# Performance work log

Hardware: AMD Instinct MI355X
Metric: run time of the kernel (lower is better)

## Reference

```python
import jax, jax.numpy as jnp
import numpy as np

N_NODES = 100000
N_EDGES = 1600000
N_GRAPHS = 256
F_IN = 38
HID = 64


def graph_conv(x, edge_index, w_rel, b_rel, w_root):
    # PyG GraphConv (aggr='add'): out = lin_rel(sum_{j in N(i)} x_j) + lin_root(x_i)
    src, dst = edge_index[0], edge_index[1]
    agg = jax.ops.segment_sum(x[src], dst, num_segments=N_NODES)  # [N, F]
    return agg @ w_rel + b_rel + x @ w_root


def setup_inputs() -> dict:
    key = jax.random.key(0)
    ks = jax.random.split(key, 10)
    x = jax.random.normal(ks[0], (N_NODES, F_IN), dtype=jnp.float32)
    edge_index = jax.random.randint(ks[1], (2, N_EDGES), 0, N_NODES, dtype=jnp.int64)
    batch = jnp.sort(jax.random.randint(ks[2], (N_NODES,), 0, N_GRAPHS, dtype=jnp.int64))
    s1 = 1.0 / np.sqrt(F_IN)
    s2 = 1.0 / np.sqrt(HID)
    w1_rel = jax.random.uniform(ks[3], (F_IN, HID), jnp.float32, -s1, s1)
    b1_rel = jax.random.uniform(ks[4], (HID,), jnp.float32, -s1, s1)
    w1_root = jax.random.uniform(ks[5], (F_IN, HID), jnp.float32, -s1, s1)
    w2_rel = jax.random.uniform(ks[6], (HID, HID), jnp.float32, -s2, s2)
    b2_rel = jax.random.uniform(ks[7], (HID,), jnp.float32, -s2, s2)
    w2_root = jax.random.uniform(ks[8], (HID, HID), jnp.float32, -s2, s2)
    return {"x": x, "edge_index": edge_index, "batch": batch,
            "w1_rel": w1_rel, "b1_rel": b1_rel, "w1_root": w1_root,
            "w2_rel": w2_rel, "b2_rel": b2_rel, "w2_root": w2_root}


def reference(x, edge_index, batch, w1_rel, b1_rel, w1_root, w2_rel, b2_rel, w2_root):
    h = graph_conv(x, edge_index, w1_rel, b1_rel, w1_root)
    h = jax.nn.relu(h)
    h = graph_conv(h, edge_index, w2_rel, b2_rel, w2_root)
    # global_mean_pool: segment mean over batch ids
    sums = jax.ops.segment_sum(h, batch, num_segments=N_GRAPHS)  # [G, HID]
    counts = jax.ops.segment_sum(jnp.ones((N_NODES,), h.dtype), batch, num_segments=N_GRAPHS)
    pooled = sums / jnp.maximum(counts, 1.0)[:, None]
    # dropout(p=0.5, training=False) is identity in eval mode
    return jax.nn.relu(pooled)
```

## Files before the change

### kernel.cpp

```cpp
#include <hip/hip_runtime.h>

#define N_NODES 100000
#define N_EDGES 1600000
#define N_GRAPHS 256
#define F_IN 38
#define F_PAD 40
#define HID 64
#define CAPD 48

#define NB   391
#define EPB  4096
#define NBLK 391
#define BCAP 4608

typedef unsigned short ushort;
typedef unsigned int uint;
typedef _Float16 h2 __attribute__((ext_vector_type(2)));

__device__ __forceinline__ h2 u2h(uint u) {
    union { uint u; h2 h; } v; v.u = u; return v.h;
}
__device__ __forceinline__ uint h2u(h2 h) {
    union { uint u; h2 h; } v; v.h = h; return v.u;
}
__device__ __forceinline__ ushort f2h_bits(float f) {
    union { _Float16 h; ushort s; } v; v.h = (_Float16)f; return v.s;
}
__device__ __forceinline__ int clampi(int v) {
    return (int)min((uint)v, (uint)N_NODES);
}

__global__ void pack_x_kernel(const float* __restrict__ x,
                              ushort* __restrict__ xb,
                              ushort* __restrict__ hb) {
    int tid = blockIdx.x * blockDim.x + threadIdx.x;
    if (tid < HID) hb[(N_NODES << 6) + tid] = 0;
    if (tid >= (N_NODES + 1) * F_PAD) return;
    int n = tid / F_PAD;
    int f = tid - n * F_PAD;
    float v = (n < N_NODES && f < F_IN) ? x[n * F_IN + f] : 0.0f;
    xb[tid] = f2h_bits(v);
}

__global__ void scatter_kernel(const int* __restrict__ src,
                               const int* __restrict__ dst,
                               int* __restrict__ gcur,
                               uint2* __restrict__ ebuf) {
    __shared__ int hist[NB];
    __shared__ int cur[NB];
    for (int i = threadIdx.x; i < NB; i += 256) hist[i] = 0;
    __syncthreads();
    const int base = blockIdx.x * EPB;
    int d[EPB / 256];
    #pragma unroll
    for (int i = 0; i < EPB / 256; ++i) {
        int e = base + i * 256 + threadIdx.x;
        d[i] = (e < N_EDGES) ? dst[e] : -1;
        if (d[i] >= 0) atomicAdd(&hist[d[i] >> 8], 1);
    }
    __syncthreads();
    for (int i = threadIdx.x; i < NB; i += 256) {
        int c = hist[i];
        cur[i] = (c > 0) ? atomicAdd(&gcur[i], c) : 0;
    }
    __syncthreads();
    #pragma unroll
    for (int i = 0; i < EPB / 256; ++i) {
        int e = base + i * 256 + threadIdx.x;
        if (d[i] >= 0) {
            int b = d[i] >> 8;
            int pos = atomicAdd(&cur[b], 1);
            if (pos < BCAP) ebuf[b * BCAP + pos] = make_uint2((uint)src[e], (uint)d[i]);
        }
    }
}

__global__ void build_kernel(const uint2* __restrict__ ebuf,
                             const int* __restrict__ gcur,
                             int* __restrict__ cnt,
                             int* __restrict__ slots) {
    __shared__ int cl[256];
    const int b = blockIdx.x;
    cl[threadIdx.x] = 0;
    __syncthreads();
    int e1 = gcur[b]; if (e1 > BCAP) e1 = BCAP;
    for (int idx = threadIdx.x; idx < e1; idx += 256) {
        uint2 e = ebuf[b * BCAP + idx];
        int pos = atomicAdd(&cl[e.y & 255], 1);
        if (pos < CAPD) slots[(int)e.y * CAPD + pos] = (int)e.x;
    }
    __syncthreads();
    int n = (b << 8) + threadIdx.x;
    if (n < N_NODES) cnt[n] = cl[threadIdx.x];
}

__global__ __launch_bounds__(256, 4) void layer1_kernel(
        const uint* __restrict__ xb32,
        const int* __restrict__ cnt,
        const int* __restrict__ slots,
        const float* __restrict__ w_rel,
        const float* __restrict__ b_rel,
        const float* __restrict__ w_root,
        const int* __restrict__ batch,
        ushort* __restrict__ hb,
        float* __restrict__ hsum) {
    __shared__ uint s_wrelp[20 * HID];
    __shared__ uint s_wrootp[20 * HID];
    __shared__ uint s_a[64][20];
    __shared__ uint s_x[64][20];
    for (int i = threadIdx.x; i < 20 * HID; i += 256) {
        int kk = i >> 6, cc = i & 63;
        int k0 = 2 * kk, k1 = 2 * kk + 1;
        float r0 = (k0 < F_IN) ? w_rel[k0 * HID + cc] : 0.f;
        float r1 = (k1 < F_IN) ? w_rel[k1 * HID + cc] : 0.f;
        float o0 = (k0 < F_IN) ? w_root[k0 * HID + cc] : 0.f;
        float o1 = (k1 < F_IN) ? w_root[k1 * HID + cc] : 0.f;
        s_wrelp[i]  = (uint)f2h_bits(r0) | ((uint)f2h_bits(r1) << 16);
        s_wrootp[i] = (uint)f2h_bits(o0) | ((uint)f2h_bits(o1) << 16);
    }
    const int wave = threadIdx.x >> 6, lane = threadIdx.x & 63;
    const int half = lane >> 5, l32 = lane & 31;
    const int base = blockIdx.x * 64;

    for (int i = 0; i < 8; ++i) {
        int nl = wave * 16 + 2 * i + half;
        int n = base + nl;
        uint xv = 0;
        int dp = 0;
        if (n < N_NODES) {
            int deg = cnt[n]; if (deg > CAPD) deg = CAPD;
            dp = (deg + 15) & ~15; if (dp > CAPD) dp = CAPD;
            if (l32 < 20) xv = xb32[n * 20 + l32];
        }
        h2 sum = {(_Float16)0, (_Float16)0};
        const int* sl = slots + n * CAPD;
        for (int j = 0; j < dp; j += 16) {
            int4 a4 = *(const int4*)(sl + j);
            int4 b4 = *(const int4*)(sl + j + 4);
            int4 c4 = *(const int4*)(sl + j + 8);
            int4 d4 = *(const int4*)(sl + j + 12);
            if (l32 < 20) {
                uint v0 = xb32[clampi(a4.x) * 20 + l32];
                uint v1 = xb32[clampi(a4.y) * 20 + l32];
                uint v2 = xb32[clampi(a4.z) * 20 + l32];
                uint v3 = xb32[clampi(a4.w) * 20 + l32];
                uint v4 = xb32[clampi(b4.x) * 20 + l32];
                uint v5 = xb32[clampi(b4.y) * 20 + l32];
                uint v6 = xb32[clampi(b4.z) * 20 + l32];
                uint v7 = xb32[clampi(b4.w) * 20 + l32];
                uint v8 = xb32[clampi(c4.x) * 20 + l32];
                uint v9 = xb32[clampi(c4.y) * 20 + l32];
                uint va = xb32[clampi(c4.z) * 20 + l32];
                uint vb = xb32[clampi(c4.w) * 20 + l32];
                uint vc = xb32[clampi(d4.x) * 20 + l32];
                uint vd = xb32[clampi(d4.y) * 20 + l32];
                uint ve = xb32[clampi(d4.z) * 20 + l32];
                uint vf = xb32[clampi(d4.w) * 20 + l32];
                h2 t0 = (u2h(v0) + u2h(v1)) + (u2h(v2) + u2h(v3));
                h2 t1 = (u2h(v4) + u2h(v5)) + (u2h(v6) + u2h(v7));
                h2 t2 = (u2h(v8) + u2h(v9)) + (u2h(va) + u2h(vb));
                h2 t3 = (u2h(vc) + u2h(vd)) + (u2h(ve) + u2h(vf));
                sum += (t0 + t1) + (t2 + t3);
            }
        }
        if (l32 < 20) {
            s_a[nl][l32] = h2u(sum);
            s_x[nl][l32] = xv;
        }
    }
    __syncthreads();

    const int c = lane, r = wave;
    const float bias = b_rel[c];
    float psum = 0.f;
    int cur_g = -1;
    for (int i = 0; i < 16; ++i) {
        int nl = r * 16 + i;
        int n = base + nl;
        if (n >= N_NODES) break;
        h2 acc = {(_Float16)0, (_Float16)0};
        #pragma unroll
        for (int k8 = 0; k8 < 5; ++k8) {
            uint4 pa = *(const uint4*)&s_a[nl][k8 * 4];
            uint4 px = *(const uint4*)&s_x[nl][k8 * 4];
            acc += u2h(pa.x) * u2h(s_wrelp[(k8 * 4 + 0) * HID + c]);
            acc += u2h(pa.y) * u2h(s_wrelp[(k8 * 4 + 1) * HID + c]);
            acc += u2h(pa.z) * u2h(s_wrelp[(k8 * 4 + 2) * HID + c]);
            acc += u2h(pa.w) * u2h(s_wrelp[(k8 * 4 + 3) * HID + c]);
            acc += u2h(px.x) * u2h(s_wrootp[(k8 * 4 + 0) * HID + c]);
            acc += u2h(px.y) * u2h(s_wrootp[(k8 * 4 + 1) * HID + c]);
            acc += u2h(px.z) * u2h(s_wrootp[(k8 * 4 + 2) * HID + c]);
            acc += u2h(px.w) * u2h(s_wrootp[(k8 * 4 + 3) * HID + c]);
        }
        float hv = fmaxf((float)acc.x + (float)acc.y + bias, 0.f);
        hb[(n << 6) + c] = f2h_bits(hv);
        int g = batch[n];
        if (g != cur_g) {
            if (cur_g >= 0) atomicAdd(&hsum[(cur_g << 6) + c], psum);
            psum = 0.f;
            cur_g = g;
        }
        psum += hv;
    }
    if (cur_g >= 0) atomicAdd(&hsum[(cur_g << 6) + c], psum);
}

__global__ __launch_bounds__(256, 4) void layer2_kernel(
        const uint* __restrict__ hb32,
        const int* __restrict__ cnt,
        const int* __restrict__ slots,
        const int* __restrict__ batch,
        float* __restrict__ esum) {
    const int wave = threadIdx.x >> 6, lane = threadIdx.x & 63;
    const int half = lane >> 5, l32 = lane & 31;
    const int base = blockIdx.x * 64;

    float psum0 = 0.f, psum1 = 0.f;
    int cur_g = -1;
    for (int i = 0; i < 8; ++i) {
        int n = base + wave * 16 + 2 * i + half;
        if (n < N_NODES) {
            int deg = cnt[n]; if (deg > CAPD) deg = CAPD;
            int dp = (deg + 15) & ~15; if (dp > CAPD) dp = CAPD;
            h2 sum = {(_Float16)0, (_Float16)0};
            const int* sl = slots + n * CAPD;
            for (int j = 0; j < dp; j += 16) {
                int4 a4 = *(const int4*)(sl + j);
                int4 b4 = *(const int4*)(sl + j + 4);
                int4 c4 = *(const int4*)(sl + j + 8);
                int4 d4 = *(const int4*)(sl + j + 12);
                uint v0 = hb32[(clampi(a4.x) << 5) + l32];
                uint v1 = hb32[(clampi(a4.y) << 5) + l32];
                uint v2 = hb32[(clampi(a4.z) << 5) + l32];
                uint v3 = hb32[(clampi(a4.w) << 5) + l32];
                uint v4 = hb32[(clampi(b4.x) << 5) + l32];
                uint v5 = hb32[(clampi(b4.y) << 5) + l32];
                uint v6 = hb32[(clampi(b4.z) << 5) + l32];
                uint v7 = hb32[(clampi(b4.w) << 5) + l32];
                uint v8 = hb32[(clampi(c4.x) << 5) + l32];
                uint v9 = hb32[(clampi(c4.y) << 5) + l32];
                uint va = hb32[(clampi(c4.z) << 5) + l32];
                uint vb = hb32[(clampi(c4.w) << 5) + l32];
                uint vc = hb32[(clampi(d4.x) << 5) + l32];
                uint vd = hb32[(clampi(d4.y) << 5) + l32];
                uint ve = hb32[(clampi(d4.z) << 5) + l32];
                uint vf = hb32[(clampi(d4.w) << 5) + l32];
                h2 t0 = (u2h(v0) + u2h(v1)) + (u2h(v2) + u2h(v3));
                h2 t1 = (u2h(v4) + u2h(v5)) + (u2h(v6) + u2h(v7));
                h2 t2 = (u2h(v8) + u2h(v9)) + (u2h(va) + u2h(vb));
                h2 t3 = (u2h(vc) + u2h(vd)) + (u2h(ve) + u2h(vf));
                sum += (t0 + t1) + (t2 + t3);
            }
            int g = batch[n];
            if (g != cur_g) {
                if (cur_g >= 0) {
                    atomicAdd(&esum[(cur_g << 6) + 2 * l32], psum0);
                    atomicAdd(&esum[(cur_g << 6) + 2 * l32 + 1], psum1);
                }
                psum0 = 0.f; psum1 = 0.f;
                cur_g = g;
            }
            psum0 += (float)sum.x;
            psum1 += (float)sum.y;
        }
    }
    if (cur_g >= 0) {
        atomicAdd(&esum[(cur_g << 6) + 2 * l32], psum0);
        atomicAdd(&esum[(cur_g << 6) + 2 * l32 + 1], psum1);
    }
}

__global__ void finalize_kernel(const float* __restrict__ esum,
                                const float* __restrict__ hsum,
                                const float* __restrict__ w2_rel,
                                const float* __restrict__ w2_root,
                                const float* __restrict__ b2,
                                const int* __restrict__ batch,
                                float* __restrict__ out) {
    __shared__ float s_e[HID];
    __shared__ float s_h[HID];
    const int g = blockIdx.x;
    const int c = threadIdx.x;
    s_e[c] = esum[(g << 6) + c];
    s_h[c] = hsum[(g << 6) + c];
    __syncthreads();

    int lo = 0, hi = N_NODES;
    while (lo < hi) { int m = (lo + hi) >> 1; if (batch[m] < g) lo = m + 1; else hi = m; }
    int start = lo;
    hi = N_NODES;
    while (lo < hi) { int m = (lo + hi) >> 1; if (batch[m] < g + 1) lo = m + 1; else hi = m; }
    int cntg = lo - start;

    float acc = (float)cntg * b2[c];
    #pragma unroll
    for (int k = 0; k < HID; ++k) {
        acc += s_e[k] * w2_rel[k * HID + c];
        acc += s_h[k] * w2_root[k * HID + c];
    }
    float denom = cntg > 0 ? (float)cntg : 1.f;
    out[(g << 6) + c] = fmaxf(acc / denom, 0.f);
}

extern "C" void kernel_launch(void* const* d_in, const int* in_sizes, int n_in,
                              void* d_out, int out_size, void* d_ws, size_t ws_size,
                              hipStream_t stream) {
    const float* x       = (const float*)d_in[0];
    const int*   ei      = (const int*)  d_in[1];
    const int*   batch   = (const int*)  d_in[2];
    const float* w1_rel  = (const float*)d_in[3];
    const float* b1_rel  = (const float*)d_in[4];
    const float* w1_root = (const float*)d_in[5];
    const float* w2_rel  = (const float*)d_in[6];
    const float* b2_rel  = (const float*)d_in[7];
    const float* w2_root = (const float*)d_in[8];
    float* out = (float*)d_out;

    const int* src = ei;
    const int* dst = ei + N_EDGES;

    char* wsb = (char*)d_ws;
    int*    cnt   = (int*)   (wsb);
    float*  hsum  = (float*) (wsb + 400000);
    float*  esum  = (float*) (wsb + 465536);
    int*    gcur  = (int*)   (wsb + 531072);
    int*    slots = (int*)   (wsb + 532640);
    ushort* xb    = (ushort*)(wsb + 19732640);
    ushort* hb    = (ushort*)(wsb + 27732720);
    uint2*  ebuf  = (uint2*) (wsb + 19732640);

    hipMemsetAsync(wsb + 400000, 0, 132636, stream);

    scatter_kernel<<<NBLK, 256, 0, stream>>>(src, dst, gcur, ebuf);
    build_kernel<<<NB, 256, 0, stream>>>(ebuf, gcur, cnt, slots);

    {
        int total = (N_NODES + 1) * F_PAD;
        pack_x_kernel<<<(total + 255) / 256, 256, 0, stream>>>(x, xb, hb);
    }
    {
        int blocks = (N_NODES + 63) / 64;
        layer1_kernel<<<blocks, 256, 0, stream>>>((const uint*)xb, cnt, slots,
                                                  w1_rel, b1_rel, w1_root, batch,
                                                  hb, hsum);
    }
    {
        int blocks = (N_NODES + 63) / 64;
        layer2_kernel<<<blocks, 256, 0, stream>>>((const uint*)hb, cnt, slots,
                                                  batch, esum);
    }
    {
        finalize_kernel<<<N_GRAPHS, HID, 0, stream>>>(esum, hsum, w2_rel, w2_root,
                                                      b2_rel, batch, out);
    }
}
```

Measured before the change: 254.5 us.

## Replace layer-2 node gather with source-bucketed edge scatter into per-graph LDS sums

Layer 2 now skips the per-node gather over dst adjacency. A second scatter pass buckets edges by source node, packing src and the destination's graph id into one word. A 1024-thread persistent kernel adds h[src] straight into per-graph shared-memory sums with LDS atomics, and the finalize step reduces the per-block partials. It also packs layer-1 edge records into one 32-bit word and pads slot lists in build. The trade is an extra scatter pass, a dense 256x64 LDS float atomic stream per block, and a 196-way partial reduction in finalize, in place of the per-node neighbor gathers.

```diff
diff --git a/kernel.cpp b/kernel.cpp
--- a/kernel.cpp
+++ b/kernel.cpp
@@ -12,6 +12,7 @@
 #define EPB  4096
 #define NBLK 391
 #define BCAP 4608
+#define P2   196
 
 typedef unsigned short ushort;
 typedef unsigned int uint;
@@ -45,18 +46,22 @@
 __global__ void scatter_kernel(const int* __restrict__ src,
                                const int* __restrict__ dst,
                                int* __restrict__ gcur,
-                               uint2* __restrict__ ebuf) {
+                               uint* __restrict__ ebuf) {
     __shared__ int hist[NB];
     __shared__ int cur[NB];
     for (int i = threadIdx.x; i < NB; i += 256) hist[i] = 0;
     __syncthreads();
     const int base = blockIdx.x * EPB;
     int d[EPB / 256];
+    uint pl[EPB / 256];
     #pragma unroll
     for (int i = 0; i < EPB / 256; ++i) {
         int e = base + i * 256 + threadIdx.x;
         d[i] = (e < N_EDGES) ? dst[e] : -1;
-        if (d[i] >= 0) atomicAdd(&hist[d[i] >> 8], 1);
+        if (d[i] >= 0) {
+            pl[i] = ((uint)src[e] << 8) | ((uint)d[i] & 255u);
+            atomicAdd(&hist[d[i] >> 8], 1);
+        }
     }
     __syncthreads();
     for (int i = threadIdx.x; i < NB; i += 256) {
@@ -66,16 +71,15 @@
     __syncthreads();
     #pragma unroll
     for (int i = 0; i < EPB / 256; ++i) {
-        int e = base + i * 256 + threadIdx.x;
         if (d[i] >= 0) {
             int b = d[i] >> 8;
             int pos = atomicAdd(&cur[b], 1);
-            if (pos < BCAP) ebuf[b * BCAP + pos] = make_uint2((uint)src[e], (uint)d[i]);
-        }
-    }
-}
-
-__global__ void build_kernel(const uint2* __restrict__ ebuf,
+            if (pos < BCAP) ebuf[b * BCAP + pos] = pl[i];
+        }
+    }
+}
+
+__global__ void build_kernel(const uint* __restrict__ ebuf,
                              const int* __restrict__ gcur,
                              int* __restrict__ cnt,
                              int* __restrict__ slots) {
@@ -85,13 +89,20 @@
     __syncthreads();
     int e1 = gcur[b]; if (e1 > BCAP) e1 = BCAP;
     for (int idx = threadIdx.x; idx < e1; idx += 256) {
-        uint2 e = ebuf[b * BCAP + idx];
-        int pos = atomicAdd(&cl[e.y & 255], 1);
-        if (pos < CAPD) slots[(int)e.y * CAPD + pos] = (int)e.x;
+        uint e = ebuf[b * BCAP + idx];
+        int dl = (int)(e & 255u);
+        int pos = atomicAdd(&cl[dl], 1);
+        if (pos < CAPD) slots[((b << 8) + dl) * CAPD + pos] = (int)(e >> 8);
     }
     __syncthreads();
     int n = (b << 8) + threadIdx.x;
-    if (n < N_NODES) cnt[n] = cl[threadIdx.x];
+    if (n < N_NODES) {
+        int c = cl[threadIdx.x];
+        cnt[n] = c;
+        int d = (c > CAPD) ? CAPD : c;
+        int dp = (d + 15) & ~15; if (dp > CAPD) dp = CAPD;
+        for (int j = d; j < dp; ++j) slots[n * CAPD + j] = N_NODES;
+    }
 }
 
 __global__ __launch_bounds__(256, 4) void layer1_kernel(
@@ -205,72 +216,82 @@
     if (cur_g >= 0) atomicAdd(&hsum[(cur_g << 6) + c], psum);
 }
 
-__global__ __launch_bounds__(256, 4) void layer2_kernel(
+__global__ void scatter2_kernel(const int* __restrict__ src,
+                                const int* __restrict__ dst,
+                                const int* __restrict__ batch,
+                                int* __restrict__ gcur2,
+                                uint* __restrict__ ebuf2) {
+    __shared__ int hist[NB];
+    __shared__ int cur[NB];
+    for (int i = threadIdx.x; i < NB; i += 256) hist[i] = 0;
+    __syncthreads();
+    const int base = blockIdx.x * EPB;
+    int sv[EPB / 256];
+    uint pl[EPB / 256];
+    #pragma unroll
+    for (int i = 0; i < EPB / 256; ++i) {
+        int e = base + i * 256 + threadIdx.x;
+        sv[i] = -1;
+        if (e < N_EDGES) {
+            int s = src[e];
+            int g = batch[dst[e]];
+            sv[i] = s;
+            pl[i] = ((uint)s << 8) | (uint)g;
+            atomicAdd(&hist[s >> 8], 1);
+        }
+    }
+    __syncthreads();
+    for (int i = threadIdx.x; i < NB; i += 256) {
+        int c = hist[i];
+        cur[i] = (c > 0) ? atomicAdd(&gcur2[i], c) : 0;
+    }
+    __syncthreads();
+    #pragma unroll
+    for (int i = 0; i < EPB / 256; ++i) {
+        if (sv[i] >= 0) {
+            int b = sv[i] >> 8;
+            int pos = atomicAdd(&cur[b], 1);
+            if (pos < BCAP) ebuf2[b * BCAP + pos] = pl[i];
+        }
+    }
+}
+
+__global__ __launch_bounds__(1024) void layer2_kernel(
         const uint* __restrict__ hb32,
-        const int* __restrict__ cnt,
-        const int* __restrict__ slots,
-        const int* __restrict__ batch,
-        float* __restrict__ esum) {
+        const uint* __restrict__ ebuf2,
+        const int* __restrict__ gcur2,
+        float* __restrict__ partial) {
+    __shared__ float s_es[N_GRAPHS * HID];
+    for (int i = threadIdx.x; i < N_GRAPHS * HID; i += 1024) s_es[i] = 0.f;
+    __syncthreads();
     const int wave = threadIdx.x >> 6, lane = threadIdx.x & 63;
     const int half = lane >> 5, l32 = lane & 31;
-    const int base = blockIdx.x * 64;
-
-    float psum0 = 0.f, psum1 = 0.f;
-    int cur_g = -1;
-    for (int i = 0; i < 8; ++i) {
-        int n = base + wave * 16 + 2 * i + half;
-        if (n < N_NODES) {
-            int deg = cnt[n]; if (deg > CAPD) deg = CAPD;
-            int dp = (deg + 15) & ~15; if (dp > CAPD) dp = CAPD;
-            h2 sum = {(_Float16)0, (_Float16)0};
-            const int* sl = slots + n * CAPD;
-            for (int j = 0; j < dp; j += 16) {
-                int4 a4 = *(const int4*)(sl + j);
-                int4 b4 = *(const int4*)(sl + j + 4);
-                int4 c4 = *(const int4*)(sl + j + 8);
-                int4 d4 = *(const int4*)(sl + j + 12);
-                uint v0 = hb32[(clampi(a4.x) << 5) + l32];
-                uint v1 = hb32[(clampi(a4.y) << 5) + l32];
-                uint v2 = hb32[(clampi(a4.z) << 5) + l32];
-                uint v3 = hb32[(clampi(a4.w) << 5) + l32];
-                uint v4 = hb32[(clampi(b4.x) << 5) + l32];
-                uint v5 = hb32[(clampi(b4.y) << 5) + l32];
-                uint v6 = hb32[(clampi(b4.z) << 5) + l32];
-                uint v7 = hb32[(clampi(b4.w) << 5) + l32];
-                uint v8 = hb32[(clampi(c4.x) << 5) + l32];
-                uint v9 = hb32[(clampi(c4.y) << 5) + l32];
-                uint va = hb32[(clampi(c4.z) << 5) + l32];
-                uint vb = hb32[(clampi(c4.w) << 5) + l32];
-                uint vc = hb32[(clampi(d4.x) << 5) + l32];
-                uint vd = hb32[(clampi(d4.y) << 5) + l32];
-                uint ve = hb32[(clampi(d4.z) << 5) + l32];
-                uint vf = hb32[(clampi(d4.w) << 5) + l32];
-                h2 t0 = (u2h(v0) + u2h(v1)) + (u2h(v2) + u2h(v3));
-                h2 t1 = (u2h(v4) + u2h(v5)) + (u2h(v6) + u2h(v7));
-                h2 t2 = (u2h(v8) + u2h(v9)) + (u2h(va) + u2h(vb));
-                h2 t3 = (u2h(vc) + u2h(vd)) + (u2h(ve) + u2h(vf));
-                sum += (t0 + t1) + (t2 + t3);
+    for (int b = blockIdx.x; b < NB; b += P2) {
+        int e1 = gcur2[b]; if (e1 > BCAP) e1 = BCAP;
+        const uint* eb = ebuf2 + b * BCAP;
+        for (int base = wave << 6; base < e1; base += 16 << 6) {
+            int cnt = e1 - base; if (cnt > 64) cnt = 64;
+            uint pv = (lane < cnt) ? eb[base + lane] : 0u;
+            #pragma unroll 4
+            for (int k = 0; k < 32; ++k) {
+                int idx2 = 2 * k + half;
+                uint p = __shfl(pv, idx2, 64);
+                if (idx2 < cnt) {
+                    int srcn = (int)(p >> 8);
+                    int g = (int)(p & 255u);
+                    h2 hv = u2h(hb32[(srcn << 5) + l32]);
+                    atomicAdd(&s_es[(g << 6) + l32],      (float)hv.x);
+                    atomicAdd(&s_es[(g << 6) + 32 + l32], (float)hv.y);
+                }
             }
-            int g = batch[n];
-            if (g != cur_g) {
-                if (cur_g >= 0) {
-                    atomicAdd(&esum[(cur_g << 6) + 2 * l32], psum0);
-                    atomicAdd(&esum[(cur_g << 6) + 2 * l32 + 1], psum1);
-                }
-                psum0 = 0.f; psum1 = 0.f;
-                cur_g = g;
-            }
-            psum0 += (float)sum.x;
-            psum1 += (float)sum.y;
-        }
-    }
-    if (cur_g >= 0) {
-        atomicAdd(&esum[(cur_g << 6) + 2 * l32], psum0);
-        atomicAdd(&esum[(cur_g << 6) + 2 * l32 + 1], psum1);
-    }
-}
-
-__global__ void finalize_kernel(const float* __restrict__ esum,
+        }
+    }
+    __syncthreads();
+    float* pp = partial + blockIdx.x * (N_GRAPHS * HID);
+    for (int i = threadIdx.x; i < N_GRAPHS * HID; i += 1024) pp[i] = s_es[i];
+}
+
+__global__ void finalize_kernel(const float* __restrict__ partial,
                                 const float* __restrict__ hsum,
                                 const float* __restrict__ w2_rel,
                                 const float* __restrict__ w2_root,
@@ -281,7 +302,11 @@
     __shared__ float s_h[HID];
     const int g = blockIdx.x;
     const int c = threadIdx.x;
-    s_e[c] = esum[(g << 6) + c];
+    int idx = (g << 6) + ((c & 1) ? 32 + (c >> 1) : (c >> 1));
+    float se = 0.f;
+    #pragma unroll 4
+    for (int p = 0; p < P2; ++p) se += partial[p * (N_GRAPHS * HID) + idx];
+    s_e[c] = se;
     s_h[c] = hsum[(g << 6) + c];
     __syncthreads();
 
@@ -320,14 +345,16 @@
     const int* dst = ei + N_EDGES;
 
     char* wsb = (char*)d_ws;
-    int*    cnt   = (int*)   (wsb);
-    float*  hsum  = (float*) (wsb + 400000);
-    float*  esum  = (float*) (wsb + 465536);
-    int*    gcur  = (int*)   (wsb + 531072);
-    int*    slots = (int*)   (wsb + 532640);
-    ushort* xb    = (ushort*)(wsb + 19732640);
-    ushort* hb    = (ushort*)(wsb + 27732720);
-    uint2*  ebuf  = (uint2*) (wsb + 19732640);
+    int*    cnt     = (int*)   (wsb);
+    float*  hsum    = (float*) (wsb + 400000);
+    int*    gcur2   = (int*)   (wsb + 465536);
+    int*    gcur    = (int*)   (wsb + 531072);
+    int*    slots   = (int*)   (wsb + 532640);
+    uint*   ebuf2   = (uint*)  (wsb + 532640);
+    float*  partial = (float*) (wsb + 7739552);
+    ushort* xb      = (ushort*)(wsb + 19732640);
+    uint*   ebuf    = (uint*)  (wsb + 19732640);
+    ushort* hb      = (ushort*)(wsb + 27732720);
 
     hipMemsetAsync(wsb + 400000, 0, 132636, stream);
 
@@ -344,13 +371,9 @@
                                                   w1_rel, b1_rel, w1_root, batch,
                                                   hb, hsum);
     }
-    {
-        int blocks = (N_NODES + 63) / 64;
-        layer2_kernel<<<blocks, 256, 0, stream>>>((const uint*)hb, cnt, slots,
-                                                  batch, esum);
-    }
-    {
-        finalize_kernel<<<N_GRAPHS, HID, 0, stream>>>(esum, hsum, w2_rel, w2_root,
-                                                      b2_rel, batch, out);
-    }
-}
+    scatter2_kernel<<<NBLK, 256, 0, stream>>>(src, dst, batch, gcur2, ebuf2);
+    layer2_kernel<<<P2, 1024, 0, stream>>>((const uint*)hb, ebuf2, gcur2, partial);
+
+    finalize_kernel<<<N_GRAPHS, HID, 0, stream>>>(partial, hsum, w2_rel, w2_root,
+                                                  b2_rel, batch, out);
+}
```

Measured after the change: 926.4 us. 3.64x slower.

## Pack edge src and local dst into one word, pre-pad slots, raise occupancy

Applied to the files above, without the earlier changes.

The scatter stage now stores each edge as a single 32-bit word (src shifted left by 8, OR'd with the low 8 bits of dst) instead of a uint2, halving edge-buffer traffic. The bucket id supplies the rest of dst when the build stage reads it. The build stage also fills padding slots up to the next multiple of 16 with the sentinel node id, so the layer kernels can read padded neighbour lists safely. The layer kernels raise their launch_bounds occupancy hint from 4 to 8, which may add register pressure or spilling.

```diff
diff --git a/kernel.cpp b/kernel.cpp
--- a/kernel.cpp
+++ b/kernel.cpp
@@ -45,18 +45,22 @@
 __global__ void scatter_kernel(const int* __restrict__ src,
                                const int* __restrict__ dst,
                                int* __restrict__ gcur,
-                               uint2* __restrict__ ebuf) {
+                               uint* __restrict__ ebuf) {
     __shared__ int hist[NB];
     __shared__ int cur[NB];
     for (int i = threadIdx.x; i < NB; i += 256) hist[i] = 0;
     __syncthreads();
     const int base = blockIdx.x * EPB;
     int d[EPB / 256];
+    uint pl[EPB / 256];
     #pragma unroll
     for (int i = 0; i < EPB / 256; ++i) {
         int e = base + i * 256 + threadIdx.x;
         d[i] = (e < N_EDGES) ? dst[e] : -1;
-        if (d[i] >= 0) atomicAdd(&hist[d[i] >> 8], 1);
+        if (d[i] >= 0) {
+            pl[i] = ((uint)src[e] << 8) | ((uint)d[i] & 255u);
+            atomicAdd(&hist[d[i] >> 8], 1);
+        }
     }
     __syncthreads();
     for (int i = threadIdx.x; i < NB; i += 256) {
@@ -66,16 +70,15 @@
     __syncthreads();
     #pragma unroll
     for (int i = 0; i < EPB / 256; ++i) {
-        int e = base + i * 256 + threadIdx.x;
         if (d[i] >= 0) {
             int b = d[i] >> 8;
             int pos = atomicAdd(&cur[b], 1);
-            if (pos < BCAP) ebuf[b * BCAP + pos] = make_uint2((uint)src[e], (uint)d[i]);
-        }
-    }
-}
-
-__global__ void build_kernel(const uint2* __restrict__ ebuf,
+            if (pos < BCAP) ebuf[b * BCAP + pos] = pl[i];
+        }
+    }
+}
+
+__global__ void build_kernel(const uint* __restrict__ ebuf,
                              const int* __restrict__ gcur,
                              int* __restrict__ cnt,
                              int* __restrict__ slots) {
@@ -85,16 +88,23 @@
     __syncthreads();
     int e1 = gcur[b]; if (e1 > BCAP) e1 = BCAP;
     for (int idx = threadIdx.x; idx < e1; idx += 256) {
-        uint2 e = ebuf[b * BCAP + idx];
-        int pos = atomicAdd(&cl[e.y & 255], 1);
-        if (pos < CAPD) slots[(int)e.y * CAPD + pos] = (int)e.x;
+        uint e = ebuf[b * BCAP + idx];
+        int dl = (int)(e & 255u);
+        int pos = atomicAdd(&cl[dl], 1);
+        if (pos < CAPD) slots[((b << 8) + dl) * CAPD + pos] = (int)(e >> 8);
     }
     __syncthreads();
     int n = (b << 8) + threadIdx.x;
-    if (n < N_NODES) cnt[n] = cl[threadIdx.x];
-}
-
-__global__ __launch_bounds__(256, 4) void layer1_kernel(
+    if (n < N_NODES) {
+        int c = cl[threadIdx.x];
+        cnt[n] = c;
+        int d = (c > CAPD) ? CAPD : c;
+        int dp = (d + 15) & ~15; if (dp > CAPD) dp = CAPD;
+        for (int j = d; j < dp; ++j) slots[n * CAPD + j] = N_NODES;
+    }
+}
+
+__global__ __launch_bounds__(256, 8) void layer1_kernel(
         const uint* __restrict__ xb32,
         const int* __restrict__ cnt,
         const int* __restrict__ slots,
@@ -205,7 +215,7 @@
     if (cur_g >= 0) atomicAdd(&hsum[(cur_g << 6) + c], psum);
 }
 
-__global__ __launch_bounds__(256, 4) void layer2_kernel(
+__global__ __launch_bounds__(256, 8) void layer2_kernel(
         const uint* __restrict__ hb32,
         const int* __restrict__ cnt,
         const int* __restrict__ slots,
@@ -327,7 +337,7 @@
     int*    slots = (int*)   (wsb + 532640);
     ushort* xb    = (ushort*)(wsb + 19732640);
     ushort* hb    = (ushort*)(wsb + 27732720);
-    uint2*  ebuf  = (uint2*) (wsb + 19732640);
+    uint*   ebuf  = (uint*)  (wsb + 19732640);
 
     hipMemsetAsync(wsb + 400000, 0, 132636, stream);
 
```

Result: no change. 256.9 us (+0.9%).

## Fuse x packing and direct atomic adjacency build into one preprocessing kernel

Applied to the files above, without the earlier changes.

Replaces the two-pass bucketed scatter/build of the adjacency slots with a single pass that uses global atomics on per-node counters to place source ids directly. That pass is merged with the x-to-fp16 packing kernel into one launch, with block ranges split by role. The memset now also clears the cnt array. Layer2 launch bounds go up to 8 blocks per SM. This removes two launches and the intermediate edge buffer round trip, but brings 1.6M scattered global atomics and less local slot write ordering, plus possible register pressure in layer2.

```diff
diff --git a/kernel.cpp b/kernel.cpp
--- a/kernel.cpp
+++ b/kernel.cpp
@@ -8,10 +8,9 @@
 #define HID 64
 #define CAPD 48
 
-#define NB   391
-#define EPB  4096
-#define NBLK 391
-#define BCAP 4608
+#define PACK_BLOCKS 15626
+#define EPB_D 4096
+#define EDGE_BLOCKS 391
 
 typedef unsigned short ushort;
 typedef unsigned int uint;
@@ -30,68 +29,34 @@
     return (int)min((uint)v, (uint)N_NODES);
 }
 
-__global__ void pack_x_kernel(const float* __restrict__ x,
-                              ushort* __restrict__ xb,
-                              ushort* __restrict__ hb) {
-    int tid = blockIdx.x * blockDim.x + threadIdx.x;
-    if (tid < HID) hb[(N_NODES << 6) + tid] = 0;
-    if (tid >= (N_NODES + 1) * F_PAD) return;
-    int n = tid / F_PAD;
-    int f = tid - n * F_PAD;
-    float v = (n < N_NODES && f < F_IN) ? x[n * F_IN + f] : 0.0f;
-    xb[tid] = f2h_bits(v);
-}
-
-__global__ void scatter_kernel(const int* __restrict__ src,
-                               const int* __restrict__ dst,
-                               int* __restrict__ gcur,
-                               uint2* __restrict__ ebuf) {
-    __shared__ int hist[NB];
-    __shared__ int cur[NB];
-    for (int i = threadIdx.x; i < NB; i += 256) hist[i] = 0;
-    __syncthreads();
-    const int base = blockIdx.x * EPB;
-    int d[EPB / 256];
-    #pragma unroll
-    for (int i = 0; i < EPB / 256; ++i) {
-        int e = base + i * 256 + threadIdx.x;
-        d[i] = (e < N_EDGES) ? dst[e] : -1;
-        if (d[i] >= 0) atomicAdd(&hist[d[i] >> 8], 1);
-    }
-    __syncthreads();
-    for (int i = threadIdx.x; i < NB; i += 256) {
-        int c = hist[i];
-        cur[i] = (c > 0) ? atomicAdd(&gcur[i], c) : 0;
-    }
-    __syncthreads();
-    #pragma unroll
-    for (int i = 0; i < EPB / 256; ++i) {
-        int e = base + i * 256 + threadIdx.x;
-        if (d[i] >= 0) {
-            int b = d[i] >> 8;
-            int pos = atomicAdd(&cur[b], 1);
-            if (pos < BCAP) ebuf[b * BCAP + pos] = make_uint2((uint)src[e], (uint)d[i]);
-        }
-    }
-}
-
-__global__ void build_kernel(const uint2* __restrict__ ebuf,
-                             const int* __restrict__ gcur,
-                             int* __restrict__ cnt,
-                             int* __restrict__ slots) {
-    __shared__ int cl[256];
+__global__ void fused_pre_kernel(const float* __restrict__ x,
+                                 const int* __restrict__ src,
+                                 const int* __restrict__ dst,
+                                 int* __restrict__ cnt,
+                                 int* __restrict__ slots,
+                                 ushort* __restrict__ xb,
+                                 ushort* __restrict__ hb) {
     const int b = blockIdx.x;
-    cl[threadIdx.x] = 0;
-    __syncthreads();
-    int e1 = gcur[b]; if (e1 > BCAP) e1 = BCAP;
-    for (int idx = threadIdx.x; idx < e1; idx += 256) {
-        uint2 e = ebuf[b * BCAP + idx];
-        int pos = atomicAdd(&cl[e.y & 255], 1);
-        if (pos < CAPD) slots[(int)e.y * CAPD + pos] = (int)e.x;
-    }
-    __syncthreads();
-    int n = (b << 8) + threadIdx.x;
-    if (n < N_NODES) cnt[n] = cl[threadIdx.x];
+    if (b < PACK_BLOCKS) {
+        int tid = b * 256 + threadIdx.x;
+        if (tid < HID) hb[(N_NODES << 6) + tid] = 0;
+        if (tid >= (N_NODES + 1) * F_PAD) return;
+        int n = tid / F_PAD;
+        int f = tid - n * F_PAD;
+        float v = (n < N_NODES && f < F_IN) ? x[n * F_IN + f] : 0.0f;
+        xb[tid] = f2h_bits(v);
+    } else {
+        const int base = (b - PACK_BLOCKS) * EPB_D + threadIdx.x;
+        #pragma unroll
+        for (int i = 0; i < EPB_D / 256; ++i) {
+            int e = base + i * 256;
+            if (e < N_EDGES) {
+                int d = dst[e];
+                int pos = atomicAdd(&cnt[d], 1);
+                if (pos < CAPD) slots[d * CAPD + pos] = src[e];
+            }
+        }
+    }
 }
 
 __global__ __launch_bounds__(256, 4) void layer1_kernel(
@@ -205,7 +170,7 @@
     if (cur_g >= 0) atomicAdd(&hsum[(cur_g << 6) + c], psum);
 }
 
-__global__ __launch_bounds__(256, 4) void layer2_kernel(
+__global__ __launch_bounds__(256, 8) void layer2_kernel(
         const uint* __restrict__ hb32,
         const int* __restrict__ cnt,
         const int* __restrict__ slots,
@@ -323,20 +288,15 @@
     int*    cnt   = (int*)   (wsb);
     float*  hsum  = (float*) (wsb + 400000);
     float*  esum  = (float*) (wsb + 465536);
-    int*    gcur  = (int*)   (wsb + 531072);
     int*    slots = (int*)   (wsb + 532640);
     ushort* xb    = (ushort*)(wsb + 19732640);
     ushort* hb    = (ushort*)(wsb + 27732720);
-    uint2*  ebuf  = (uint2*) (wsb + 19732640);
-
-    hipMemsetAsync(wsb + 400000, 0, 132636, stream);
-
-    scatter_kernel<<<NBLK, 256, 0, stream>>>(src, dst, gcur, ebuf);
-    build_kernel<<<NB, 256, 0, stream>>>(ebuf, gcur, cnt, slots);
+
+    hipMemsetAsync(wsb, 0, 531072, stream);
 
     {
-        int total = (N_NODES + 1) * F_PAD;
-        pack_x_kernel<<<(total + 255) / 256, 256, 0, stream>>>(x, xb, hb);
+        fused_pre_kernel<<<PACK_BLOCKS + EDGE_BLOCKS, 256, 0, stream>>>(
+            x, src, dst, cnt, slots, xb, hb);
     }
     {
         int blocks = (N_NODES + 63) / 64;
```

After: 309.2 us. +21.5%, slower.
